# Optimization experiments

Hardware: AMD Instinct MI355X
Metric: run time of the kernel (lower is better)

Reference implementation:

```python
import jax, jax.numpy as jnp
import numpy as np

DIM = 2048
K_DIM = 2048
Q_HEADS = 16
KV_HEADS = 4
HEAD_DIM = DIM // Q_HEADS  # 128
KV_DIM = HEAD_DIM * KV_HEADS
ROPE_THETA = 10000.0


def _rope_cos_sin(seq_len, head_dim):
    inv = 1.0 / (ROPE_THETA ** (np.arange(0, head_dim, 2).astype(np.float32) / head_dim))
    t = np.arange(seq_len, dtype=np.float32)
    freqs = np.outer(t, inv)  # (n, head_dim/2)
    return jnp.asarray(np.cos(freqs)), jnp.asarray(np.sin(freqs))


def _apply_rope(x, cos, sin):
    # x: (b, n, h, d); interleaved complex pairs as in torch.view_as_complex
    b, n, h, d = x.shape
    xr, xi = x[..., 0::2], x[..., 1::2]
    c = cos[None, :, None, :]
    s = sin[None, :, None, :]
    yr = xr * c - xi * s
    yi = xr * s + xi * c
    return jnp.stack([yr, yi], axis=-1).reshape(b, n, h, d)


def setup_inputs() -> dict:
    key = jax.random.key(0)
    ks = jax.random.split(key, 11)
    B, N = 2, 2048
    std_q = DIM ** -0.5
    std_k = K_DIM ** -0.5
    return {
        "query": jax.random.normal(ks[0], (B, N, DIM), jnp.float32),
        "key": jax.random.normal(ks[1], (B, N, K_DIM), jnp.float32),
        "value": jax.random.normal(ks[2], (B, N, K_DIM), jnp.float32),
        "Wq": jax.random.normal(ks[3], (DIM, DIM), jnp.float32) * std_q,
        "bq": jnp.zeros((DIM,), jnp.float32),
        "Wk": jax.random.normal(ks[4], (KV_DIM, K_DIM), jnp.float32) * std_k,
        "bk": jnp.zeros((KV_DIM,), jnp.float32),
        "Wv": jax.random.normal(ks[5], (KV_DIM, K_DIM), jnp.float32) * std_k,
        "bv": jnp.zeros((KV_DIM,), jnp.float32),
        "Wo": jax.random.normal(ks[6], (DIM, DIM), jnp.float32) * std_q,
        "bo": jnp.zeros((DIM,), jnp.float32),
    }


def reference(query, key, value, Wq, bq, Wk, bk, Wv, bv, Wo, bo):
    b, nq, _ = query.shape
    nk = key.shape[1]
    q = (query @ Wq.T + bq).reshape(b, nq, Q_HEADS, HEAD_DIM)
    k = (key @ Wk.T + bk).reshape(b, nk, KV_HEADS, HEAD_DIM)
    v = (value @ Wv.T + bv).reshape(b, nk, KV_HEADS, HEAD_DIM)
    cos, sin = _rope_cos_sin(max(nq, nk), HEAD_DIM)
    q = _apply_rope(q, cos[:nq], sin[:nq])
    k = _apply_rope(k, cos[:nk], sin[:nk])
    g = Q_HEADS // KV_HEADS
    # group query heads: head index hh = h*g + gi uses kv head h
    qg = q.reshape(b, nq, KV_HEADS, g, HEAD_DIM)
    scale = HEAD_DIM ** -0.5
    scores = jnp.einsum('bnhgd,bshd->bhgns', qg, k) * scale
    causal = jnp.tril(jnp.ones((nq, nk), dtype=bool))
    scores = jnp.where(causal, scores, jnp.finfo(scores.dtype).min)
    attn = jax.nn.softmax(scores, axis=-1)
    out = jnp.einsum('bhgns,bshd->bnhgd', attn, v).reshape(b, nq, DIM)
    return out @ Wo.T + bo
```

## Files before the change

kernel.cpp:

```cpp
#include <hip/hip_runtime.h>
#include <hip/hip_bf16.h>
#include <stdint.h>

typedef unsigned short u16;
typedef __bf16 v8bf __attribute__((ext_vector_type(8)));
typedef float f32x4 __attribute__((ext_vector_type(4)));

#define BATCH 2
#define NSEQ  2048
#define DIM_  2048
#define QH    16
#define KVH   4
#define HD    128
#define KVDIM 512
#define QKVS  3072
#define MROWS (BATCH*NSEQ)

__device__ __forceinline__ u16 f2bf(float f) {
  uint32_t u = __builtin_bit_cast(uint32_t, f);
  u += 0x7FFFu + ((u >> 16) & 1u);
  return (u16)(u >> 16);
}
__device__ __forceinline__ float bf2f(u16 h) {
  uint32_t u = ((uint32_t)h) << 16;
  return __builtin_bit_cast(float, u);
}
__device__ __forceinline__ uint32_t cvt_pk_bf16(float lo, float hi) {
  uint32_t r;
  asm("v_cvt_pk_bf16_f32 %0, %1, %2" : "=v"(r) : "v"(lo), "v"(hi));
  return r;
}
__device__ __forceinline__ void gload_lds16(const void* g, void* l) {
  __builtin_amdgcn_global_load_lds((const __attribute__((address_space(1))) void*)g,
                                   (__attribute__((address_space(3))) void*)l, 16, 0, 0);
}

__global__ void k_conv_w(const float* __restrict__ wq, const float* __restrict__ wk,
                         const float* __restrict__ wv, const float* __restrict__ wo,
                         u16* __restrict__ oq, u16* __restrict__ ok,
                         u16* __restrict__ ov, u16* __restrict__ oo) {
  int i = (blockIdx.x * 256 + threadIdx.x) * 4;
  const float* in; u16* out; int e;
  if (i < 4194304)      { in = wq; out = oq; e = i; }
  else if (i < 5242880) { in = wk; out = ok; e = i - 4194304; }
  else if (i < 6291456) { in = wv; out = ov; e = i - 5242880; }
  else                  { in = wo; out = oo; e = i - 6291456; }
  float4 v = *(const float4*)(in + e);
  ushort4 o;
  o.x = f2bf(v.x); o.y = f2bf(v.y); o.z = f2bf(v.z); o.w = f2bf(v.w);
  *(ushort4*)(out + e) = o;
}

__global__ void k_conv_x(const float* __restrict__ q, const float* __restrict__ k,
                         const float* __restrict__ v,
                         u16* __restrict__ oq, u16* __restrict__ ok, u16* __restrict__ ov) {
  int i = (blockIdx.x * 256 + threadIdx.x) * 4;
  int r = i >> 23;
  int e = i & ((1 << 23) - 1);
  const float* in = (r == 0) ? q : (r == 1 ? k : v);
  u16* out = (r == 0) ? oq : (r == 1 ? ok : ov);
  float4 vv = *(const float4*)(in + e);
  ushort4 o;
  o.x = f2bf(vv.x); o.y = f2bf(vv.y); o.z = f2bf(vv.z); o.w = f2bf(vv.w);
  *(ushort4*)(out + e) = o;
}

__global__ void k_rope_table2(float2* __restrict__ tab) {
  int idx = blockIdx.x * 256 + threadIdx.x;
  if (idx < NSEQ * 64) {
    int i = idx & 63;
    float inv = powf(10000.0f, -(float)i / 64.0f);
    float ang = (float)(idx >> 6) * inv;
    tab[idx] = make_float2(cosf(ang), sinf(ang));
  }
}

__global__ void k_transpose_v(const u16* __restrict__ vp, u16* __restrict__ vt) {
  size_t idx = (size_t)blockIdx.x * 256 + threadIdx.x;
  if (idx >= (size_t)BATCH * KVH * HD * NSEQ) return;
  int n = (int)(idx & (NSEQ - 1));
  int d = (int)((idx >> 11) & (HD - 1));
  int h = (int)((idx >> 18) & (KVH - 1));
  int b = (int)(idx >> 20);
  vt[idx] = vp[(size_t)(b * NSEQ + n) * QKVS + h * HD + d];
}

__global__ __launch_bounds__(256) void k_gemm_qkv(const u16* __restrict__ xq, const u16* __restrict__ xk,
                                                  const u16* __restrict__ xv,
                                                  const u16* __restrict__ wq, const u16* __restrict__ wk,
                                                  const u16* __restrict__ wv,
                                                  const float* __restrict__ bq, const float* __restrict__ bk,
                                                  const float* __restrict__ bv,
                                                  const float2* __restrict__ tab2, u16* __restrict__ C) {
  __shared__ __align__(16) u16 As[2][128 * 32];
  __shared__ __align__(16) u16 Bs[2][128 * 32];
  int tid = threadIdx.x;
  int l = tid & 63, w = tid >> 6;
  int lg = l >> 4, lr = l & 15;
  int wr = w >> 1, wc = w & 1;
  int bm = blockIdx.x, bn = blockIdx.y;

  const u16* A; const u16* B; const float* bias;
  if (bn < 16)      { A = xq; B = wq + (size_t)(bn * 128) * 2048;        bias = bq + bn * 128; }
  else if (bn < 20) { A = xk; B = wk + (size_t)((bn - 16) * 128) * 2048; bias = bk + (bn - 16) * 128; }
  else              { A = xv; B = wv + (size_t)((bn - 20) * 128) * 2048; bias = bv + (bn - 20) * 128; }

  int srow = tid >> 2;
  int scol = (tid & 3) * 16;

  const char* Ab = (const char*)A + ((size_t)(bm * 128 + srow) * 2048) * 2 + scol;
  const char* Bb = (const char*)B + ((size_t)srow * 2048) * 2 + scol;

#define STG(BUF, KT)                                                            \
  {                                                                             \
    size_t koff = (size_t)(KT) * 64;                                            \
    gload_lds16(Ab + koff, (char*)As[BUF] + srow * 64 + scol);                  \
    gload_lds16(Ab + koff + (size_t)64 * 2048 * 2,                              \
                (char*)As[BUF] + (srow + 64) * 64 + scol);                      \
    gload_lds16(Bb + koff, (char*)Bs[BUF] + srow * 64 + scol);                  \
    gload_lds16(Bb + koff + (size_t)64 * 2048 * 2,                              \
                (char*)Bs[BUF] + (srow + 64) * 64 + scol);                      \
  }

  f32x4 acc[4][4] = {};
  STG(0, 0);
  __syncthreads();
  for (int kt = 0; kt < 64; ++kt) {
    int cur = kt & 1;
    if (kt < 63) STG(cur ^ 1, kt + 1);
    const char* AsB = (const char*)As[cur];
    const char* BsB = (const char*)Bs[cur];
    v8bf af[4], bfr[4];
#pragma unroll
    for (int mi = 0; mi < 4; ++mi)
      af[mi] = *(const v8bf*)(AsB + (wr * 64 + mi * 16 + lr) * 64 + lg * 16);
#pragma unroll
    for (int ni = 0; ni < 4; ++ni)
      bfr[ni] = *(const v8bf*)(BsB + (wc * 64 + ni * 16 + lr) * 64 + lg * 16);
#pragma unroll
    for (int mi = 0; mi < 4; ++mi)
#pragma unroll
      for (int ni = 0; ni < 4; ++ni)
        acc[mi][ni] = __builtin_amdgcn_mfma_f32_16x16x32_bf16(af[mi], bfr[ni], acc[mi][ni], 0, 0, 0);
    __syncthreads();
  }
#undef STG

  bool rope = (bn < 20);
#pragma unroll
  for (int mi = 0; mi < 4; ++mi)
#pragma unroll
    for (int ni = 0; ni < 4; ++ni) {
      int grow0 = bm * 128 + wr * 64 + mi * 16 + lg * 4;
      int lcol = wc * 64 + ni * 16 + lr;
      int gcol = bn * 128 + lcol;
      float bsv = bias[lcol];
      if (rope) {
        int i2 = (gcol & 127) >> 1;
#pragma unroll
        for (int r = 0; r < 4; ++r) {
          float v = acc[mi][ni][r] + bsv;
          float pv = __shfl_xor(v, 1);
          int t = (grow0 + r) & (NSEQ - 1);
          float2 cs = tab2[t * 64 + i2];
          float y = (lr & 1) ? (pv * cs.y + v * cs.x) : (v * cs.x - pv * cs.y);
          C[(size_t)(grow0 + r) * QKVS + gcol] = f2bf(y);
        }
      } else {
#pragma unroll
        for (int r = 0; r < 4; ++r)
          C[(size_t)(grow0 + r) * QKVS + gcol] = f2bf(acc[mi][ni][r] + bsv);
      }
    }
}

__global__ __launch_bounds__(256) void k_gemm_bt(const u16* __restrict__ A, const u16* __restrict__ B,
                                                 const float* __restrict__ bias, float* __restrict__ C,
                                                 int M, int N, int K) {
  __shared__ __align__(16) u16 As[2][128 * 32];
  __shared__ __align__(16) u16 Bs[2][128 * 32];
  int tid = threadIdx.x;
  int l = tid & 63, w = tid >> 6;
  int lg = l >> 4, lr = l & 15;
  int wr = w >> 1, wc = w & 1;
  int bm = blockIdx.x, bn = blockIdx.y;

  int srow = tid >> 2;
  int scol = (tid & 3) * 16;

  const char* Ab = (const char*)A + ((size_t)(bm * 128 + srow) * K) * 2 + scol;
  const char* Bb = (const char*)B + ((size_t)(bn * 128 + srow) * K) * 2 + scol;

#define STG(BUF, KT)                                                            \
  {                                                                             \
    size_t koff = (size_t)(KT) * 64;                                            \
    gload_lds16(Ab + koff, (char*)As[BUF] + srow * 64 + scol);                  \
    gload_lds16(Ab + koff + (size_t)64 * K * 2,                                 \
                (char*)As[BUF] + (srow + 64) * 64 + scol);                      \
    gload_lds16(Bb + koff, (char*)Bs[BUF] + srow * 64 + scol);                  \
    gload_lds16(Bb + koff + (size_t)64 * K * 2,                                 \
                (char*)Bs[BUF] + (srow + 64) * 64 + scol);                      \
  }

  f32x4 acc[4][4] = {};
  int ksteps = K >> 5;
  STG(0, 0);
  __syncthreads();
  for (int kt = 0; kt < ksteps; ++kt) {
    int cur = kt & 1;
    if (kt + 1 < ksteps) STG(cur ^ 1, kt + 1);
    const char* AsB = (const char*)As[cur];
    const char* BsB = (const char*)Bs[cur];
    v8bf af[4], bfr[4];
#pragma unroll
    for (int mi = 0; mi < 4; ++mi)
      af[mi] = *(const v8bf*)(AsB + (wr * 64 + mi * 16 + lr) * 64 + lg * 16);
#pragma unroll
    for (int ni = 0; ni < 4; ++ni)
      bfr[ni] = *(const v8bf*)(BsB + (wc * 64 + ni * 16 + lr) * 64 + lg * 16);
#pragma unroll
    for (int mi = 0; mi < 4; ++mi)
#pragma unroll
      for (int ni = 0; ni < 4; ++ni)
        acc[mi][ni] = __builtin_amdgcn_mfma_f32_16x16x32_bf16(af[mi], bfr[ni], acc[mi][ni], 0, 0, 0);
    __syncthreads();
  }
#undef STG

#pragma unroll
  for (int mi = 0; mi < 4; ++mi)
#pragma unroll
    for (int ni = 0; ni < 4; ++ni) {
      int grow0 = bm * 128 + wr * 64 + mi * 16 + lg * 4;
      int gcol = bn * 128 + wc * 64 + ni * 16 + lr;
      float bsv = bias[gcol];
#pragma unroll
      for (int r = 0; r < 4; ++r)
        C[(size_t)(grow0 + r) * N + gcol] = acc[mi][ni][r] + bsv;
    }
}

__global__ __launch_bounds__(256, 2) void k_attn(const u16* __restrict__ q, const u16* __restrict__ k,
                                                 const u16* __restrict__ vt, u16* __restrict__ out) {
  __shared__ __align__(16) u16 Ks[64 * 128];
  __shared__ __align__(16) u16 Vs[128 * 64];

  int tid = threadIdx.x;
  int l = tid & 63, w = tid >> 6;
  int lg = l >> 4, lr = l & 15;
  int h = blockIdx.y, b = blockIdx.z;
  int kvh = h >> 2;
  const float SCL2 = 0.12752551286084109f;
  const float THR2 = 11.541560327111708f;

  const char* kbase = (const char*)k + ((size_t)(b * NSEQ) * QKVS + kvh * HD) * 2;
  const char* vbase = (const char*)vt + ((size_t)(b * KVH + kvh) * HD) * NSEQ * 2;
  char* KsB = (char*)Ks;
  char* VsB = (char*)Vs;

  int krow0 = tid >> 4;
  int kcol = (tid & 15) * 16;
  int vrow0 = tid >> 3;
  int vcol = (tid & 7) * 16;

  v8bf kr[4], vr[4];

#define LOADKV(KT)                                                                          \
  {                                                                                         \
    _Pragma("unroll") for (int i = 0; i < 4; ++i)                                           \
        kr[i] = *(const v8bf*)(kbase + (size_t)((KT) * 64 + krow0 + i * 16) * QKVS * 2 + kcol); \
    _Pragma("unroll") for (int i = 0; i < 4; ++i)                                           \
        vr[i] = *(const v8bf*)(vbase + (size_t)(vrow0 + i * 32) * NSEQ * 2 + (size_t)(KT) * 128 + vcol); \
  }
#define WRITEKV()                                                                           \
  {                                                                                         \
    _Pragma("unroll") for (int i = 0; i < 4; ++i) {                                         \
      int kvl = krow0 + i * 16;                                                             \
      int prow = (kvl & 32) + ((kvl & 4) << 2) + ((kvl & 24) >> 1) + (kvl & 3);             \
      *(v8bf*)(KsB + prow * 256 + (kcol ^ ((prow & 7) << 4))) = kr[i];                      \
    }                                                                                       \
    _Pragma("unroll") for (int i = 0; i < 4; ++i) {                                         \
      int row = vrow0 + i * 32;                                                             \
      *(v8bf*)(VsB + row * 128 + (vcol ^ ((row & 7) << 4))) = vr[i];                        \
    }                                                                                       \
  }

  for (int pass = 0; pass < 2; ++pass) {
    int qt = pass ? (31 - blockIdx.x) : blockIdx.x;
    int q0 = qt * 64 + w * 16;

    const char* qb = (const char*)q + ((size_t)(b * NSEQ + q0 + lr) * QKVS + h * HD) * 2;
    v8bf qf[4];
#pragma unroll
    for (int kk = 0; kk < 4; ++kk) qf[kk] = *(const v8bf*)(qb + kk * 64 + lg * 16);

    f32x4 od[8] = {};
    float m2 = -INFINITY, lsum = 0.f;
    int qrow = q0 + lr;

    int ktmax = qt;
    LOADKV(0);
    WRITEKV();
    __syncthreads();

    for (int kt = 0; kt <= ktmax; ++kt) {
      if (kt < ktmax) LOADKV(kt + 1);

      f32x4 st[4];
      __builtin_amdgcn_s_setprio(1);
#pragma unroll
      for (int nt = 0; nt < 4; ++nt) {
        f32x4 a = {};
#pragma unroll
        for (int kk = 0; kk < 4; ++kk) {
          int krow = nt * 16 + lr;
          v8bf kf = *(const v8bf*)(KsB + krow * 256 + ((kk * 64 + lg * 16) ^ ((krow & 7) << 4)));
          a = __builtin_amdgcn_mfma_f32_16x16x32_bf16(kf, qf[kk], a, 0, 0, 0);
        }
        st[nt] = a;
      }
      __builtin_amdgcn_s_setprio(0);

      float mx = -1e30f;
#pragma unroll
      for (int nt = 0; nt < 4; ++nt)
#pragma unroll
        for (int r = 0; r < 4; ++r) {
          int kv = kt * 64 + (nt >> 1) * 32 + lg * 8 + ((nt & 1) << 2) + r;
          float v = st[nt][r] * SCL2;
          if (kv > qrow) v = -1e30f;
          st[nt][r] = v;
          mx = fmaxf(mx, v);
        }
      mx = fmaxf(mx, __shfl_xor(mx, 16));
      mx = fmaxf(mx, __shfl_xor(mx, 32));

      if (!__all(mx - m2 <= THR2)) {
        float nm2 = fmaxf(m2, mx);
        float corrf = exp2f(m2 - nm2);
        m2 = nm2;
        lsum *= corrf;
#pragma unroll
        for (int r = 0; r < 4; ++r) {
          float cb = __shfl(corrf, lg * 4 + r);
#pragma unroll
          for (int dt = 0; dt < 8; ++dt) od[dt][r] *= cb;
        }
      }

      float rs = 0.f;
#pragma unroll
      for (int nt = 0; nt < 4; ++nt)
#pragma unroll
        for (int r = 0; r < 4; ++r) {
          float pv = exp2f(st[nt][r] - m2);
          st[nt][r] = pv;
          rs += pv;
        }
      rs += __shfl_xor(rs, 16);
      rs += __shfl_xor(rs, 32);
      lsum += rs;

      uint32_t pk[4][2];
#pragma unroll
      for (int nt = 0; nt < 4; ++nt)
#pragma unroll
        for (int s = 0; s < 2; ++s)
          pk[nt][s] = cvt_pk_bf16(st[nt][2 * s], st[nt][2 * s + 1]);

      __builtin_amdgcn_s_setprio(1);
#pragma unroll
      for (int kc = 0; kc < 2; ++kc) {
        union { uint32_t u[4]; v8bf v; } pfu;
        pfu.u[0] = pk[2 * kc][0];
        pfu.u[1] = pk[2 * kc][1];
        pfu.u[2] = pk[2 * kc + 1][0];
        pfu.u[3] = pk[2 * kc + 1][1];
#pragma unroll
        for (int dt = 0; dt < 8; ++dt) {
          int vrow = dt * 16 + lr;
          v8bf vf = *(const v8bf*)(VsB + vrow * 128 + ((kc * 64 + lg * 16) ^ ((vrow & 7) << 4)));
          od[dt] = __builtin_amdgcn_mfma_f32_16x16x32_bf16(pfu.v, vf, od[dt], 0, 0, 0);
        }
      }
      __builtin_amdgcn_s_setprio(0);

      __syncthreads();
      if (kt < ktmax) WRITEKV();
      __syncthreads();
    }

#pragma unroll
    for (int r = 0; r < 4; ++r) {
      float ls = __shfl(lsum, lg * 4 + r);
      float inv = 1.0f / ls;
      int qr = q0 + lg * 4 + r;
      char* ob = (char*)out + ((size_t)(b * NSEQ + qr) * DIM_ + h * HD) * 2;
#pragma unroll
      for (int dt = 0; dt < 8; ++dt)
        *(u16*)(ob + (dt * 16 + lr) * 2) = f2bf(od[dt][r] * inv);
    }
  }
#undef LOADKV
#undef WRITEKV
}

extern "C" void kernel_launch(void* const* d_in, const int* in_sizes, int n_in,
                              void* d_out, int out_size, void* d_ws, size_t ws_size,
                              hipStream_t stream) {
  const float* query = (const float*)d_in[0];
  const float* key_ = (const float*)d_in[1];
  const float* value = (const float*)d_in[2];
  const float* Wq = (const float*)d_in[3];
  const float* bq = (const float*)d_in[4];
  const float* Wk = (const float*)d_in[5];
  const float* bk = (const float*)d_in[6];
  const float* Wv = (const float*)d_in[7];
  const float* bv = (const float*)d_in[8];
  const float* Wo = (const float*)d_in[9];
  const float* bo = (const float*)d_in[10];

  char* ws = (char*)d_ws;
  u16* wq_bf = (u16*)(ws + 0);
  u16* wk_bf = (u16*)(ws + 8388608);
  u16* wv_bf = (u16*)(ws + 10485760);
  u16* wo_bf = (u16*)(ws + 12582912);
  float2* tab2 = (float2*)(ws + 20971520);
  u16* xq = (u16*)(ws + 22020096);
  u16* xk = (u16*)(ws + 38797312);
  u16* xv = (u16*)(ws + 55574528);
  u16* qkvproj = (u16*)(ws + 72351744);
  u16* vt = xq;
  u16* attno = xk;

  k_conv_w<<<dim3(10240), 256, 0, stream>>>(Wq, Wk, Wv, Wo, wq_bf, wk_bf, wv_bf, wo_bf);
  k_conv_x<<<dim3(24576), 256, 0, stream>>>(query, key_, value, xq, xk, xv);
  k_rope_table2<<<dim3(NSEQ * 64 / 256), 256, 0, stream>>>(tab2);

  k_gemm_qkv<<<dim3(MROWS / 128, QKVS / 128), 256, 0, stream>>>(xq, xk, xv, wq_bf, wk_bf, wv_bf,
                                                                bq, bk, bv, tab2, qkvproj);

  k_transpose_v<<<dim3((BATCH * KVH * HD * NSEQ) / 256), 256, 0, stream>>>(qkvproj + 2560, vt);

  k_attn<<<dim3(NSEQ / 128, QH, BATCH), 256, 0, stream>>>(qkvproj, qkvproj + 2048, vt, attno);

  k_gemm_bt<<<dim3(MROWS / 128, DIM_ / 128), 256, 0, stream>>>(attno, wo_bf, bo, (float*)d_out, MROWS, DIM_, DIM_);
}
```

Measured before the change: 248.9 us.

## Replace projection GEMMs with 256x256-tile, 8-wave, XOR-swizzled pipelined kernels

Both projection GEMMs (QKV with fused RoPE, and the output projection) move from 128x128 tiles with 4 waves to 256x256 tiles with 8 waves, a 64-wide K step and double-buffered LDS. LDS rows are XOR-swizzled and loads are staged piecewise across compute phases, with explicit vmcnt waits, barriers, sched_barrier and setprio. Block IDs are remapped for L2 locality. The aim is more data reuse per byte loaded and better overlap of global loads with MFMA work. The cost is larger LDS use, more register pressure, and fewer blocks (192 and 128), which may underfill the GPU's compute units.

```diff
diff --git a/kernel.cpp b/kernel.cpp
--- a/kernel.cpp
+++ b/kernel.cpp
@@ -85,158 +85,161 @@
   vt[idx] = vp[(size_t)(b * NSEQ + n) * QKVS + h * HD + d];
 }
 
-__global__ __launch_bounds__(256) void k_gemm_qkv(const u16* __restrict__ xq, const u16* __restrict__ xk,
-                                                  const u16* __restrict__ xv,
-                                                  const u16* __restrict__ wq, const u16* __restrict__ wk,
-                                                  const u16* __restrict__ wv,
-                                                  const float* __restrict__ bq, const float* __restrict__ bk,
-                                                  const float* __restrict__ bv,
-                                                  const float2* __restrict__ tab2, u16* __restrict__ C) {
-  __shared__ __align__(16) u16 As[2][128 * 32];
-  __shared__ __align__(16) u16 Bs[2][128 * 32];
+
+#define STG_A(T, QM)                                                              \
+  { _Pragma("unroll") for (int h_ = 0; h_ < 2; ++h_) {                            \
+      int r_ = l >> 3;                                                            \
+      const char* s_ = Ab + (size_t)(grow0 + h_ * 128 + (QM) * 64 + w * 8 + r_) * 4096 \
+                       + (size_t)(T) * 128 + (((l & 7) ^ r_) << 4);               \
+      gload_lds16(s_, (char*)&Als[(T) & 1][h_][(QM) * 64 + w * 8][0]);            \
+    } }
+
+#define STG_B(T, H)                                                               \
+  { _Pragma("unroll") for (int q_ = 0; q_ < 2; ++q_) {                            \
+      int r_ = l >> 3;                                                            \
+      const char* s_ = Bb + (size_t)(gcol0l + (H) * 128 + q_ * 64 + w * 8 + r_) * 4096 \
+                       + (size_t)(T) * 128 + (((l & 7) ^ r_) << 4);               \
+      gload_lds16(s_, (char*)&Bls[(T) & 1][H][q_ * 64 + w * 8][0]);               \
+    } }
+
+#define WAIT2 asm volatile("s_waitcnt vmcnt(2)" ::: "memory");
+#define WAIT0 asm volatile("s_waitcnt vmcnt(0)" ::: "memory");
+#define WAIT8 asm volatile("s_waitcnt vmcnt(8)" ::: "memory");
+
+#define PH(BUF, QM, QN, STAGE, WAITCODE)                                          \
+  {                                                                               \
+    v8bf af_[4][2], bf_[2][2];                                                    \
+    _Pragma("unroll") for (int mi = 0; mi < 4; ++mi)                              \
+      _Pragma("unroll") for (int ks = 0; ks < 2; ++ks)                            \
+        af_[mi][ks] = *(const v8bf*)((const char*)&Als[BUF][wr][0][0] +           \
+            ((QM) * 64 + mi * 16 + lr) * 128 +                                    \
+            ((ks * 64 + lg * 16) ^ ((lr & 7) << 4)));                             \
+    _Pragma("unroll") for (int ni = 0; ni < 2; ++ni)                              \
+      _Pragma("unroll") for (int ks = 0; ks < 2; ++ks)                            \
+        bf_[ni][ks] = *(const v8bf*)((const char*)&Bls[BUF][wc >> 1][0][0] +      \
+            (((wc & 1) * 64 + (QN) * 32 + ni * 16 + lr)) * 128 +                  \
+            ((ks * 64 + lg * 16) ^ ((lr & 7) << 4)));                             \
+    STAGE                                                                         \
+    __builtin_amdgcn_s_barrier();                                                 \
+    asm volatile("s_waitcnt lgkmcnt(0)" ::: "memory");                            \
+    __builtin_amdgcn_sched_barrier(0);                                            \
+    __builtin_amdgcn_s_setprio(1);                                                \
+    _Pragma("unroll") for (int mi = 0; mi < 4; ++mi)                              \
+      _Pragma("unroll") for (int ni = 0; ni < 2; ++ni)                            \
+        _Pragma("unroll") for (int ks = 0; ks < 2; ++ks)                          \
+          acc[(QM) * 4 + mi][(QN) * 2 + ni] = __builtin_amdgcn_mfma_f32_16x16x32_bf16( \
+              af_[mi][ks], bf_[ni][ks], acc[(QM) * 4 + mi][(QN) * 2 + ni], 0, 0, 0); \
+    __builtin_amdgcn_s_setprio(0);                                                \
+    WAITCODE                                                                      \
+    __builtin_amdgcn_s_barrier();                                                 \
+  }
+
+#define GEMM8_LOOP                                                                \
+  f32x4 acc[8][4] = {};                                                           \
+  STG_A(0, 0) STG_A(0, 1) STG_B(0, 0) STG_B(0, 1)                                 \
+  STG_A(1, 0) STG_A(1, 1) STG_B(1, 0) STG_B(1, 1)                                 \
+  WAIT8                                                                           \
+  __builtin_amdgcn_s_barrier();                                                   \
+  for (int i = 0; i < 16; ++i) {                                                  \
+    int t0 = 2 * i, t1 = 2 * i + 1;                                               \
+    bool nl = (i < 15);                                                           \
+    PH(0, 0, 0, { if (i) STG_A(t1, 1) }, {})                                      \
+    PH(0, 0, 1, { if (i) STG_B(t1, 0) }, {})                                      \
+    PH(0, 1, 0, { if (i) STG_B(t1, 1) if (nl) STG_A(t0 + 2, 0) }, {})             \
+    PH(0, 1, 1, {}, { if (nl) { WAIT2 } else { WAIT0 } })                         \
+    PH(1, 0, 0, { if (nl) STG_A(t0 + 2, 1) }, {})                                 \
+    PH(1, 0, 1, { if (nl) STG_B(t0 + 2, 0) }, {})                                 \
+    PH(1, 1, 0, { if (nl) STG_B(t0 + 2, 1) }, {})                                 \
+    PH(1, 1, 1, { if (nl) STG_A(t0 + 3, 0) }, { if (nl) WAIT2 })                  \
+  }
+
+__global__ __launch_bounds__(512, 2) void k_gemm_qkv8(
+    const u16* __restrict__ xq, const u16* __restrict__ xk, const u16* __restrict__ xv,
+    const u16* __restrict__ wq, const u16* __restrict__ wk, const u16* __restrict__ wv,
+    const float* __restrict__ bq, const float* __restrict__ bk, const float* __restrict__ bv,
+    const float2* __restrict__ tab2, u16* __restrict__ C) {
+  __shared__ __align__(16) u16 Als[2][2][128][64];
+  __shared__ __align__(16) u16 Bls[2][2][128][64];
   int tid = threadIdx.x;
   int l = tid & 63, w = tid >> 6;
   int lg = l >> 4, lr = l & 15;
-  int wr = w >> 1, wc = w & 1;
-  int bm = blockIdx.x, bn = blockIdx.y;
-
-  const u16* A; const u16* B; const float* bias;
-  if (bn < 16)      { A = xq; B = wq + (size_t)(bn * 128) * 2048;        bias = bq + bn * 128; }
-  else if (bn < 20) { A = xk; B = wk + (size_t)((bn - 16) * 128) * 2048; bias = bk + (bn - 16) * 128; }
-  else              { A = xv; B = wv + (size_t)((bn - 20) * 128) * 2048; bias = bv + (bn - 20) * 128; }
-
-  int srow = tid >> 2;
-  int scol = (tid & 3) * 16;
-
-  const char* Ab = (const char*)A + ((size_t)(bm * 128 + srow) * 2048) * 2 + scol;
-  const char* Bb = (const char*)B + ((size_t)srow * 2048) * 2 + scol;
-
-#define STG(BUF, KT)                                                            \
-  {                                                                             \
-    size_t koff = (size_t)(KT) * 64;                                            \
-    gload_lds16(Ab + koff, (char*)As[BUF] + srow * 64 + scol);                  \
-    gload_lds16(Ab + koff + (size_t)64 * 2048 * 2,                              \
-                (char*)As[BUF] + (srow + 64) * 64 + scol);                      \
-    gload_lds16(Bb + koff, (char*)Bs[BUF] + srow * 64 + scol);                  \
-    gload_lds16(Bb + koff + (size_t)64 * 2048 * 2,                              \
-                (char*)Bs[BUF] + (srow + 64) * 64 + scol);                      \
-  }
-
-  f32x4 acc[4][4] = {};
-  STG(0, 0);
-  __syncthreads();
-  for (int kt = 0; kt < 64; ++kt) {
-    int cur = kt & 1;
-    if (kt < 63) STG(cur ^ 1, kt + 1);
-    const char* AsB = (const char*)As[cur];
-    const char* BsB = (const char*)Bs[cur];
-    v8bf af[4], bfr[4];
-#pragma unroll
-    for (int mi = 0; mi < 4; ++mi)
-      af[mi] = *(const v8bf*)(AsB + (wr * 64 + mi * 16 + lr) * 64 + lg * 16);
-#pragma unroll
-    for (int ni = 0; ni < 4; ++ni)
-      bfr[ni] = *(const v8bf*)(BsB + (wc * 64 + ni * 16 + lr) * 64 + lg * 16);
-#pragma unroll
-    for (int mi = 0; mi < 4; ++mi)
-#pragma unroll
-      for (int ni = 0; ni < 4; ++ni)
-        acc[mi][ni] = __builtin_amdgcn_mfma_f32_16x16x32_bf16(af[mi], bfr[ni], acc[mi][ni], 0, 0, 0);
-    __syncthreads();
-  }
-#undef STG
-
-  bool rope = (bn < 20);
-#pragma unroll
-  for (int mi = 0; mi < 4; ++mi)
-#pragma unroll
-    for (int ni = 0; ni < 4; ++ni) {
-      int grow0 = bm * 128 + wr * 64 + mi * 16 + lg * 4;
-      int lcol = wc * 64 + ni * 16 + lr;
-      int gcol = bn * 128 + lcol;
+  int wr = w >> 2, wc = w & 3;
+
+  int bid = blockIdx.x;
+  int swz = (bid & 7) * 24 + (bid >> 3);
+  int bm = swz & 15, bn = swz >> 4;
+
+  const u16* A; const u16* Bw; const float* bias; int bnl;
+  if (bn < 8)       { A = xq; Bw = wq; bnl = bn;      bias = bq; }
+  else if (bn < 10) { A = xk; Bw = wk; bnl = bn - 8;  bias = bk; }
+  else              { A = xv; Bw = wv; bnl = bn - 10; bias = bv; }
+  int grow0 = bm * 256;
+  int gcol0l = bnl * 256;
+  const char* Ab = (const char*)A;
+  const char* Bb = (const char*)Bw;
+
+  GEMM8_LOOP
+
+  bool rope = (bn < 10);
+#pragma unroll
+  for (int fm = 0; fm < 8; ++fm)
+#pragma unroll
+    for (int fn = 0; fn < 4; ++fn) {
+      int grow = bm * 256 + wr * 128 + fm * 16 + lg * 4;
+      int lcol = bnl * 256 + wc * 64 + fn * 16 + lr;
+      int gcol = bn * 256 + wc * 64 + fn * 16 + lr;
       float bsv = bias[lcol];
       if (rope) {
         int i2 = (gcol & 127) >> 1;
 #pragma unroll
         for (int r = 0; r < 4; ++r) {
-          float v = acc[mi][ni][r] + bsv;
+          float v = acc[fm][fn][r] + bsv;
           float pv = __shfl_xor(v, 1);
-          int t = (grow0 + r) & (NSEQ - 1);
+          int t = (grow + r) & (NSEQ - 1);
           float2 cs = tab2[t * 64 + i2];
           float y = (lr & 1) ? (pv * cs.y + v * cs.x) : (v * cs.x - pv * cs.y);
-          C[(size_t)(grow0 + r) * QKVS + gcol] = f2bf(y);
+          C[(size_t)(grow + r) * QKVS + gcol] = f2bf(y);
         }
       } else {
 #pragma unroll
         for (int r = 0; r < 4; ++r)
-          C[(size_t)(grow0 + r) * QKVS + gcol] = f2bf(acc[mi][ni][r] + bsv);
+          C[(size_t)(grow + r) * QKVS + gcol] = f2bf(acc[fm][fn][r] + bsv);
       }
     }
 }
 
-__global__ __launch_bounds__(256) void k_gemm_bt(const u16* __restrict__ A, const u16* __restrict__ B,
-                                                 const float* __restrict__ bias, float* __restrict__ C,
-                                                 int M, int N, int K) {
-  __shared__ __align__(16) u16 As[2][128 * 32];
-  __shared__ __align__(16) u16 Bs[2][128 * 32];
+__global__ __launch_bounds__(512, 2) void k_gemm_bt8(const u16* __restrict__ Ain,
+                                                     const u16* __restrict__ Bw,
+                                                     const float* __restrict__ bias,
+                                                     float* __restrict__ C) {
+  __shared__ __align__(16) u16 Als[2][2][128][64];
+  __shared__ __align__(16) u16 Bls[2][2][128][64];
   int tid = threadIdx.x;
   int l = tid & 63, w = tid >> 6;
   int lg = l >> 4, lr = l & 15;
-  int wr = w >> 1, wc = w & 1;
-  int bm = blockIdx.x, bn = blockIdx.y;
-
-  int srow = tid >> 2;
-  int scol = (tid & 3) * 16;
-
-  const char* Ab = (const char*)A + ((size_t)(bm * 128 + srow) * K) * 2 + scol;
-  const char* Bb = (const char*)B + ((size_t)(bn * 128 + srow) * K) * 2 + scol;
-
-#define STG(BUF, KT)                                                            \
-  {                                                                             \
-    size_t koff = (size_t)(KT) * 64;                                            \
-    gload_lds16(Ab + koff, (char*)As[BUF] + srow * 64 + scol);                  \
-    gload_lds16(Ab + koff + (size_t)64 * K * 2,                                 \
-                (char*)As[BUF] + (srow + 64) * 64 + scol);                      \
-    gload_lds16(Bb + koff, (char*)Bs[BUF] + srow * 64 + scol);                  \
-    gload_lds16(Bb + koff + (size_t)64 * K * 2,                                 \
-                (char*)Bs[BUF] + (srow + 64) * 64 + scol);                      \
-  }
-
-  f32x4 acc[4][4] = {};
-  int ksteps = K >> 5;
-  STG(0, 0);
-  __syncthreads();
-  for (int kt = 0; kt < ksteps; ++kt) {
-    int cur = kt & 1;
-    if (kt + 1 < ksteps) STG(cur ^ 1, kt + 1);
-    const char* AsB = (const char*)As[cur];
-    const char* BsB = (const char*)Bs[cur];
-    v8bf af[4], bfr[4];
-#pragma unroll
-    for (int mi = 0; mi < 4; ++mi)
-      af[mi] = *(const v8bf*)(AsB + (wr * 64 + mi * 16 + lr) * 64 + lg * 16);
-#pragma unroll
-    for (int ni = 0; ni < 4; ++ni)
-      bfr[ni] = *(const v8bf*)(BsB + (wc * 64 + ni * 16 + lr) * 64 + lg * 16);
-#pragma unroll
-    for (int mi = 0; mi < 4; ++mi)
-#pragma unroll
-      for (int ni = 0; ni < 4; ++ni)
-        acc[mi][ni] = __builtin_amdgcn_mfma_f32_16x16x32_bf16(af[mi], bfr[ni], acc[mi][ni], 0, 0, 0);
-    __syncthreads();
-  }
-#undef STG
-
-#pragma unroll
-  for (int mi = 0; mi < 4; ++mi)
-#pragma unroll
-    for (int ni = 0; ni < 4; ++ni) {
-      int grow0 = bm * 128 + wr * 64 + mi * 16 + lg * 4;
-      int gcol = bn * 128 + wc * 64 + ni * 16 + lr;
+  int wr = w >> 2, wc = w & 3;
+
+  int bid = blockIdx.x;
+  int swz = (bid & 7) * 16 + (bid >> 3);
+  int bm = swz & 15, bn = swz >> 4;
+
+  int grow0 = bm * 256;
+  int gcol0l = bn * 256;
+  const char* Ab = (const char*)Ain;
+  const char* Bb = (const char*)Bw;
+
+  GEMM8_LOOP
+
+#pragma unroll
+  for (int fm = 0; fm < 8; ++fm)
+#pragma unroll
+    for (int fn = 0; fn < 4; ++fn) {
+      int grow = bm * 256 + wr * 128 + fm * 16 + lg * 4;
+      int gcol = bn * 256 + wc * 64 + fn * 16 + lr;
       float bsv = bias[gcol];
 #pragma unroll
       for (int r = 0; r < 4; ++r)
-        C[(size_t)(grow0 + r) * N + gcol] = acc[mi][ni][r] + bsv;
+        C[(size_t)(grow + r) * DIM_ + gcol] = acc[fm][fn][r] + bsv;
     }
 }
 
@@ -437,12 +440,12 @@
   k_conv_x<<<dim3(24576), 256, 0, stream>>>(query, key_, value, xq, xk, xv);
   k_rope_table2<<<dim3(NSEQ * 64 / 256), 256, 0, stream>>>(tab2);
 
-  k_gemm_qkv<<<dim3(MROWS / 128, QKVS / 128), 256, 0, stream>>>(xq, xk, xv, wq_bf, wk_bf, wv_bf,
-                                                                bq, bk, bv, tab2, qkvproj);
+  k_gemm_qkv8<<<dim3(192), 512, 0, stream>>>(xq, xk, xv, wq_bf, wk_bf, wv_bf,
+                                             bq, bk, bv, tab2, qkvproj);
 
   k_transpose_v<<<dim3((BATCH * KVH * HD * NSEQ) / 256), 256, 0, stream>>>(qkvproj + 2560, vt);
 
   k_attn<<<dim3(NSEQ / 128, QH, BATCH), 256, 0, stream>>>(qkvproj, qkvproj + 2048, vt, attno);
 
-  k_gemm_bt<<<dim3(MROWS / 128, DIM_ / 128), 256, 0, stream>>>(attno, wo_bf, bo, (float*)d_out, MROWS, DIM_, DIM_);
-}
+  k_gemm_bt8<<<dim3(128), 512, 0, stream>>>(attno, wo_bf, bo, (float*)d_out);
+}
```

Result: slower. 290.8 us (+16.9%).

## Fuse fp32-to-bf16 activation conversion into QKV GEMM A-tile loading

Applied to the files above, without the earlier changes.

Removes the separate k_conv_x pass that converted query/key/value to bf16. The QKV GEMM now reads fp32 activations straight into registers, converts them to bf16 and writes them to LDS after the MFMA step, which software-pipelines the next tile. This avoids writing and re-reading about 50MB of bf16 intermediates and one kernel launch. In exchange, each GEMM block reads the A tile at twice the width, and the same activations are reconverted once per N-tile across 24 column blocks. It also adds register pressure and synchronous LDS stores in place of async global-to-LDS loads.

```diff
diff --git a/kernel.cpp b/kernel.cpp
--- a/kernel.cpp
+++ b/kernel.cpp
@@ -51,20 +51,6 @@
   *(ushort4*)(out + e) = o;
 }
 
-__global__ void k_conv_x(const float* __restrict__ q, const float* __restrict__ k,
-                         const float* __restrict__ v,
-                         u16* __restrict__ oq, u16* __restrict__ ok, u16* __restrict__ ov) {
-  int i = (blockIdx.x * 256 + threadIdx.x) * 4;
-  int r = i >> 23;
-  int e = i & ((1 << 23) - 1);
-  const float* in = (r == 0) ? q : (r == 1 ? k : v);
-  u16* out = (r == 0) ? oq : (r == 1 ? ok : ov);
-  float4 vv = *(const float4*)(in + e);
-  ushort4 o;
-  o.x = f2bf(vv.x); o.y = f2bf(vv.y); o.z = f2bf(vv.z); o.w = f2bf(vv.w);
-  *(ushort4*)(out + e) = o;
-}
-
 __global__ void k_rope_table2(float2* __restrict__ tab) {
   int idx = blockIdx.x * 256 + threadIdx.x;
   if (idx < NSEQ * 64) {
@@ -85,8 +71,8 @@
   vt[idx] = vp[(size_t)(b * NSEQ + n) * QKVS + h * HD + d];
 }
 
-__global__ __launch_bounds__(256) void k_gemm_qkv(const u16* __restrict__ xq, const u16* __restrict__ xk,
-                                                  const u16* __restrict__ xv,
+__global__ __launch_bounds__(256) void k_gemm_qkv(const float* __restrict__ qin, const float* __restrict__ kin,
+                                                  const float* __restrict__ vin,
                                                   const u16* __restrict__ wq, const u16* __restrict__ wk,
                                                   const u16* __restrict__ wv,
                                                   const float* __restrict__ bq, const float* __restrict__ bk,
@@ -100,34 +86,52 @@
   int wr = w >> 1, wc = w & 1;
   int bm = blockIdx.x, bn = blockIdx.y;
 
-  const u16* A; const u16* B; const float* bias;
-  if (bn < 16)      { A = xq; B = wq + (size_t)(bn * 128) * 2048;        bias = bq + bn * 128; }
-  else if (bn < 20) { A = xk; B = wk + (size_t)((bn - 16) * 128) * 2048; bias = bk + (bn - 16) * 128; }
-  else              { A = xv; B = wv + (size_t)((bn - 20) * 128) * 2048; bias = bv + (bn - 20) * 128; }
+  const float* Af; const u16* B; const float* bias;
+  if (bn < 16)      { Af = qin; B = wq + (size_t)(bn * 128) * 2048;        bias = bq + bn * 128; }
+  else if (bn < 20) { Af = kin; B = wk + (size_t)((bn - 16) * 128) * 2048; bias = bk + (bn - 16) * 128; }
+  else              { Af = vin; B = wv + (size_t)((bn - 20) * 128) * 2048; bias = bv + (bn - 20) * 128; }
 
   int srow = tid >> 2;
   int scol = (tid & 3) * 16;
 
-  const char* Ab = (const char*)A + ((size_t)(bm * 128 + srow) * 2048) * 2 + scol;
   const char* Bb = (const char*)B + ((size_t)srow * 2048) * 2 + scol;
 
-#define STG(BUF, KT)                                                            \
-  {                                                                             \
-    size_t koff = (size_t)(KT) * 64;                                            \
-    gload_lds16(Ab + koff, (char*)As[BUF] + srow * 64 + scol);                  \
-    gload_lds16(Ab + koff + (size_t)64 * 2048 * 2,                              \
-                (char*)As[BUF] + (srow + 64) * 64 + scol);                      \
-    gload_lds16(Bb + koff, (char*)Bs[BUF] + srow * 64 + scol);                  \
-    gload_lds16(Bb + koff + (size_t)64 * 2048 * 2,                              \
-                (char*)Bs[BUF] + (srow + 64) * 64 + scol);                      \
+  float4 ar0, ar1, ar2, ar3;
+
+#define LOADA(KT)                                                                \
+  {                                                                              \
+    size_t aoff = (size_t)(bm * 128 + srow) * 2048 + (size_t)(KT) * 32 + (tid & 3) * 8; \
+    ar0 = *(const float4*)(Af + aoff);                                           \
+    ar1 = *(const float4*)(Af + aoff + 4);                                       \
+    ar2 = *(const float4*)(Af + aoff + 131072);                                  \
+    ar3 = *(const float4*)(Af + aoff + 131076);                                  \
+  }
+#define WRITEA(BUF)                                                              \
+  {                                                                              \
+    uint4 w0, w1;                                                                \
+    w0.x = cvt_pk_bf16(ar0.x, ar0.y); w0.y = cvt_pk_bf16(ar0.z, ar0.w);          \
+    w0.z = cvt_pk_bf16(ar1.x, ar1.y); w0.w = cvt_pk_bf16(ar1.z, ar1.w);          \
+    w1.x = cvt_pk_bf16(ar2.x, ar2.y); w1.y = cvt_pk_bf16(ar2.z, ar2.w);          \
+    w1.z = cvt_pk_bf16(ar3.x, ar3.y); w1.w = cvt_pk_bf16(ar3.z, ar3.w);          \
+    *(uint4*)((char*)As[BUF] + srow * 64 + scol) = w0;                           \
+    *(uint4*)((char*)As[BUF] + (srow + 64) * 64 + scol) = w1;                    \
+  }
+#define STG_B(BUF, KT)                                                           \
+  {                                                                              \
+    size_t koff = (size_t)(KT) * 64;                                             \
+    gload_lds16(Bb + koff, (char*)Bs[BUF] + srow * 64 + scol);                   \
+    gload_lds16(Bb + koff + (size_t)64 * 2048 * 2,                               \
+                (char*)Bs[BUF] + (srow + 64) * 64 + scol);                       \
   }
 
   f32x4 acc[4][4] = {};
-  STG(0, 0);
+  LOADA(0);
+  STG_B(0, 0);
+  WRITEA(0);
   __syncthreads();
   for (int kt = 0; kt < 64; ++kt) {
     int cur = kt & 1;
-    if (kt < 63) STG(cur ^ 1, kt + 1);
+    if (kt < 63) { LOADA(kt + 1); STG_B(cur ^ 1, kt + 1); }
     const char* AsB = (const char*)As[cur];
     const char* BsB = (const char*)Bs[cur];
     v8bf af[4], bfr[4];
@@ -142,9 +146,12 @@
 #pragma unroll
       for (int ni = 0; ni < 4; ++ni)
         acc[mi][ni] = __builtin_amdgcn_mfma_f32_16x16x32_bf16(af[mi], bfr[ni], acc[mi][ni], 0, 0, 0);
+    if (kt < 63) WRITEA(cur ^ 1);
     __syncthreads();
   }
-#undef STG
+#undef LOADA
+#undef WRITEA
+#undef STG_B
 
   bool rope = (bn < 20);
 #pragma unroll
@@ -426,18 +433,15 @@
   u16* wv_bf = (u16*)(ws + 10485760);
   u16* wo_bf = (u16*)(ws + 12582912);
   float2* tab2 = (float2*)(ws + 20971520);
-  u16* xq = (u16*)(ws + 22020096);
-  u16* xk = (u16*)(ws + 38797312);
-  u16* xv = (u16*)(ws + 55574528);
+  u16* vt = (u16*)(ws + 22020096);
+  u16* attno = (u16*)(ws + 38797312);
   u16* qkvproj = (u16*)(ws + 72351744);
-  u16* vt = xq;
-  u16* attno = xk;
 
   k_conv_w<<<dim3(10240), 256, 0, stream>>>(Wq, Wk, Wv, Wo, wq_bf, wk_bf, wv_bf, wo_bf);
-  k_conv_x<<<dim3(24576), 256, 0, stream>>>(query, key_, value, xq, xk, xv);
   k_rope_table2<<<dim3(NSEQ * 64 / 256), 256, 0, stream>>>(tab2);
 
-  k_gemm_qkv<<<dim3(MROWS / 128, QKVS / 128), 256, 0, stream>>>(xq, xk, xv, wq_bf, wk_bf, wv_bf,
+  k_gemm_qkv<<<dim3(MROWS / 128, QKVS / 128), 256, 0, stream>>>(query, key_, value,
+                                                                wq_bf, wk_bf, wv_bf,
                                                                 bq, bk, bv, tab2, qkvproj);
 
   k_transpose_v<<<dim3((BATCH * KVH * HD * NSEQ) / 256), 256, 0, stream>>>(qkvproj + 2560, vt);
```

Measured after the change: 227.7 us. 1.09x faster.

## Tile V transpose through LDS and widen attention blocks to 128 query rows

Applied to the files above, without the earlier changes.

The V transpose changes from a per-element strided gather to a 64x64 tile staged through shared memory, so both global reads and writes are coalesced. The attention kernel moves to 512-thread blocks covering 128 query rows, so each K/V tile loaded into LDS is shared by eight waves instead of four. This halves the K/V traffic per query row and the number of blocks. In exchange, the tighter launch bounds raise register pressure, and the first-half waves do extra fully-masked work on the last K tile.

```diff
diff --git a/kernel.cpp b/kernel.cpp
--- a/kernel.cpp
+++ b/kernel.cpp
@@ -75,14 +75,37 @@
   }
 }
 
-__global__ void k_transpose_v(const u16* __restrict__ vp, u16* __restrict__ vt) {
-  size_t idx = (size_t)blockIdx.x * 256 + threadIdx.x;
-  if (idx >= (size_t)BATCH * KVH * HD * NSEQ) return;
-  int n = (int)(idx & (NSEQ - 1));
-  int d = (int)((idx >> 11) & (HD - 1));
-  int h = (int)((idx >> 18) & (KVH - 1));
-  int b = (int)(idx >> 20);
-  vt[idx] = vp[(size_t)(b * NSEQ + n) * QKVS + h * HD + d];
+__global__ __launch_bounds__(256) void k_transpose_v(const u16* __restrict__ vp, u16* __restrict__ vt) {
+  __shared__ u16 t[64][72];
+  int bn = blockIdx.x, bd = blockIdx.y;
+  int tid = threadIdx.x;
+  int rrow = tid >> 3;
+  int rcol = (tid & 7) * 8;
+#pragma unroll
+  for (int i = 0; i < 2; ++i) {
+    int n = rrow + i * 32;
+    ushort4 v0 = *(const ushort4*)(vp + (size_t)(bn * 64 + n) * QKVS + bd * 64 + rcol);
+    ushort4 v1 = *(const ushort4*)(vp + (size_t)(bn * 64 + n) * QKVS + bd * 64 + rcol + 4);
+    *(ushort4*)&t[n][rcol] = v0;
+    *(ushort4*)&t[n][rcol + 4] = v1;
+  }
+  __syncthreads();
+  int b = bn >> 5;
+  int nbase = (bn & 31) * 64;
+#pragma unroll
+  for (int i = 0; i < 2; ++i) {
+    int dl = rrow + i * 32;
+    int dglob = bd * 64 + dl;
+    int kvh = dglob >> 7, dd = dglob & 127;
+    ushort4 o0, o1;
+    o0.x = t[rcol + 0][dl]; o0.y = t[rcol + 1][dl];
+    o0.z = t[rcol + 2][dl]; o0.w = t[rcol + 3][dl];
+    o1.x = t[rcol + 4][dl]; o1.y = t[rcol + 5][dl];
+    o1.z = t[rcol + 6][dl]; o1.w = t[rcol + 7][dl];
+    u16* dst = vt + (((size_t)(b * KVH + kvh) * HD + dd) * NSEQ + nbase + rcol);
+    *(ushort4*)dst = o0;
+    *(ushort4*)(dst + 4) = o1;
+  }
 }
 
 __global__ __launch_bounds__(256) void k_gemm_qkv(const u16* __restrict__ xq, const u16* __restrict__ xk,
@@ -240,7 +263,7 @@
     }
 }
 
-__global__ __launch_bounds__(256, 2) void k_attn(const u16* __restrict__ q, const u16* __restrict__ k,
+__global__ __launch_bounds__(512, 2) void k_attn(const u16* __restrict__ q, const u16* __restrict__ k,
                                                  const u16* __restrict__ vt, u16* __restrict__ out) {
   __shared__ __align__(16) u16 Ks[64 * 128];
   __shared__ __align__(16) u16 Vs[128 * 64];
@@ -263,31 +286,31 @@
   int vrow0 = tid >> 3;
   int vcol = (tid & 7) * 16;
 
-  v8bf kr[4], vr[4];
+  v8bf kr[2], vr[2];
 
 #define LOADKV(KT)                                                                          \
   {                                                                                         \
-    _Pragma("unroll") for (int i = 0; i < 4; ++i)                                           \
-        kr[i] = *(const v8bf*)(kbase + (size_t)((KT) * 64 + krow0 + i * 16) * QKVS * 2 + kcol); \
-    _Pragma("unroll") for (int i = 0; i < 4; ++i)                                           \
-        vr[i] = *(const v8bf*)(vbase + (size_t)(vrow0 + i * 32) * NSEQ * 2 + (size_t)(KT) * 128 + vcol); \
+    _Pragma("unroll") for (int i = 0; i < 2; ++i)                                           \
+        kr[i] = *(const v8bf*)(kbase + (size_t)((KT) * 64 + krow0 + i * 32) * QKVS * 2 + kcol); \
+    _Pragma("unroll") for (int i = 0; i < 2; ++i)                                           \
+        vr[i] = *(const v8bf*)(vbase + (size_t)(vrow0 + i * 64) * NSEQ * 2 + (size_t)(KT) * 128 + vcol); \
   }
 #define WRITEKV()                                                                           \
   {                                                                                         \
-    _Pragma("unroll") for (int i = 0; i < 4; ++i) {                                         \
-      int kvl = krow0 + i * 16;                                                             \
+    _Pragma("unroll") for (int i = 0; i < 2; ++i) {                                         \
+      int kvl = krow0 + i * 32;                                                             \
       int prow = (kvl & 32) + ((kvl & 4) << 2) + ((kvl & 24) >> 1) + (kvl & 3);             \
       *(v8bf*)(KsB + prow * 256 + (kcol ^ ((prow & 7) << 4))) = kr[i];                      \
     }                                                                                       \
-    _Pragma("unroll") for (int i = 0; i < 4; ++i) {                                         \
-      int row = vrow0 + i * 32;                                                             \
+    _Pragma("unroll") for (int i = 0; i < 2; ++i) {                                         \
+      int row = vrow0 + i * 64;                                                             \
       *(v8bf*)(VsB + row * 128 + (vcol ^ ((row & 7) << 4))) = vr[i];                        \
     }                                                                                       \
   }
 
   for (int pass = 0; pass < 2; ++pass) {
-    int qt = pass ? (31 - blockIdx.x) : blockIdx.x;
-    int q0 = qt * 64 + w * 16;
+    int qt = pass ? (15 - blockIdx.x) : blockIdx.x;
+    int q0 = qt * 128 + w * 16;
 
     const char* qb = (const char*)q + ((size_t)(b * NSEQ + q0 + lr) * QKVS + h * HD) * 2;
     v8bf qf[4];
@@ -298,7 +321,7 @@
     float m2 = -INFINITY, lsum = 0.f;
     int qrow = q0 + lr;
 
-    int ktmax = qt;
+    int ktmax = 2 * qt + 1;
     LOADKV(0);
     WRITEKV();
     __syncthreads();
@@ -440,9 +463,9 @@
   k_gemm_qkv<<<dim3(MROWS / 128, QKVS / 128), 256, 0, stream>>>(xq, xk, xv, wq_bf, wk_bf, wv_bf,
                                                                 bq, bk, bv, tab2, qkvproj);
 
-  k_transpose_v<<<dim3((BATCH * KVH * HD * NSEQ) / 256), 256, 0, stream>>>(qkvproj + 2560, vt);
-
-  k_attn<<<dim3(NSEQ / 128, QH, BATCH), 256, 0, stream>>>(qkvproj, qkvproj + 2048, vt, attno);
+  k_transpose_v<<<dim3(MROWS / 64, KVDIM / 64), 256, 0, stream>>>(qkvproj + 2560, vt);
+
+  k_attn<<<dim3(8, QH, BATCH), 512, 0, stream>>>(qkvproj, qkvproj + 2048, vt, attno);
 
   k_gemm_bt<<<dim3(MROWS / 128, DIM_ / 128), 256, 0, stream>>>(attno, wo_bf, bo, (float*)d_out, MROWS, DIM_, DIM_);
 }
```

Result: faster. 238.2 us (-4.3%).
